# Kernel optimization log

Measured on AMD Instinct MI355X. Metric: run time of the kernel, lower is better.

The kernel has to match this reference:

```python
import jax, jax.numpy as jnp
import numpy as np

BLOCK = (4, 8, 8)   # (t, h, w)
NH, D, DA = 8, 512, 64
EPS = 1e-5


def _layernorm(x, g, b):
    m = jnp.mean(x, axis=-1, keepdims=True)
    xc = x - m
    v = jnp.mean(xc * xc, axis=-1, keepdims=True)
    return xc * jax.lax.rsqrt(v + EPS) * g + b


def setup_inputs() -> dict:
    key = jax.random.key(0)
    ks = jax.random.split(key, 10)
    B, T, H, W = 2, 8, 32, 32
    t, h, w = BLOCK
    s_qkv = (2.0 / (D + DA)) ** 0.5   # xavier_normal for (d, da) fan
    s_lin = (2.0 / (D + D)) ** 0.5
    return {
        "x": jax.random.normal(ks[0], (B, D, T, H, W), jnp.float32),
        "dt_bank": 0.02 * jax.random.normal(ks[1], (NH, 2 * t - 1), jnp.float32),
        "dh_bank": 0.02 * jax.random.normal(ks[2], (NH, 2 * h - 1), jnp.float32),
        "dw_bank": 0.02 * jax.random.normal(ks[3], (NH, 2 * w - 1), jnp.float32),
        "ln1_g": jnp.ones((D,), jnp.float32),
        "ln1_b": jnp.zeros((D,), jnp.float32),
        "w_q": s_qkv * jax.random.normal(ks[4], (NH, D, DA), jnp.float32),
        "w_k": s_qkv * jax.random.normal(ks[5], (NH, D, DA), jnp.float32),
        "w_v": s_qkv * jax.random.normal(ks[6], (NH, D, DA), jnp.float32),
        "w_proj": s_lin * jax.random.normal(ks[7], (D, NH * DA), jnp.float32),
        "ln2_g": jnp.ones((D,), jnp.float32),
        "ln2_b": jnp.zeros((D,), jnp.float32),
        "w1": s_lin * jax.random.normal(ks[8], (D, D), jnp.float32),
        "b1": jnp.zeros((D,), jnp.float32),
        "w2": s_lin * jax.random.normal(ks[9], (D, D), jnp.float32),
        "b2": jnp.zeros((D,), jnp.float32),
    }


def _axial_bias(dt_bank, dh_bank, dw_bank):
    t, h, w = BLOCK
    thw = t * h * w
    ar = jnp.arange(thw)
    tt = ar // (h * w)
    hh = (ar // w) % h
    ww = ar % w
    # relative offsets shifted to be non-negative (matches dt += abs(dt.min()))
    it = tt[:, None] - tt[None, :] + (t - 1)
    ih = hh[:, None] - hh[None, :] + (h - 1)
    iw = ww[:, None] - ww[None, :] + (w - 1)
    return dt_bank[:, it] + dh_bank[:, ih] + dw_bank[:, iw]  # (NH, thw, thw)


def reference(x, dt_bank, dh_bank, dw_bank, ln1_g, ln1_b, w_q, w_k, w_v,
              w_proj, ln2_g, ln2_b, w1, b1, w2, b2):
    B, C, T, H, W = x.shape
    t, h, w = BLOCK
    st, sh, sw = T // t, H // h, W // w
    thw = t * h * w
    nb = B * st * sh * sw

    # block split: (B,C,T,H,W) -> (nb, thw, C)
    xb = x.reshape(B, C, st, t, sh, h, sw, w).transpose(0, 2, 4, 6, 1, 3, 5, 7)
    xb = xb.reshape(nb, C, thw).transpose(0, 2, 1)

    Bb = _axial_bias(dt_bank, dh_bank, dw_bank)  # (NH, thw, thw)

    # --- multi-head attention with additive axial bias ---
    resid = xb
    xn = _layernorm(xb, ln1_g, ln1_b)
    q = jnp.einsum('bnd,hde->hbne', xn, w_q)
    k = jnp.einsum('bnd,hde->hbne', xn, w_k)
    v = jnp.einsum('bnd,hde->hbne', xn, w_v)
    scale = 1.0 / jnp.sqrt(jnp.asarray(DA, x.dtype))
    attn = jnp.einsum('hbne,hbme->hbnm', q, k) * scale + Bb[:, None]
    attn = jax.nn.softmax(attn, axis=-1)
    out = jnp.einsum('hbnm,hbme->hbne', attn, v)         # (NH, nb, thw, DA)
    out = out.transpose(1, 2, 0, 3).reshape(nb, thw, NH * DA)  # head-major concat
    out = out @ w_proj.T + resid

    # --- FFN with residual ---
    y = _layernorm(out, ln2_g, ln2_b)
    y = jax.nn.relu(y @ w1.T + b1) @ w2.T + b2
    out = y + out

    # un-block: (nb, thw, C) -> (B,C,T,H,W)
    out = out.transpose(0, 2, 1).reshape(B, st, sh, sw, C, t, h, w)
    out = out.transpose(0, 4, 1, 5, 2, 6, 3, 7).reshape(B, C, T, H, W)
    return out
```

## Files before the change

### kernel.cpp

```cpp
#include <hip/hip_runtime.h>
#include <hip/hip_bf16.h>
#include <stdint.h>

typedef __attribute__((ext_vector_type(4))) float f32x4;
typedef __attribute__((ext_vector_type(8))) short s16x8;
typedef __attribute__((ext_vector_type(4))) short s16x4;
typedef __attribute__((ext_vector_type(8))) __bf16 b16x8;

__device__ __forceinline__ f32x4 mfma16(s16x8 a, s16x8 b, f32x4 c) {
  return __builtin_amdgcn_mfma_f32_16x16x32_bf16(
      __builtin_bit_cast(b16x8, a), __builtin_bit_cast(b16x8, b), c, 0, 0, 0);
}

__device__ __forceinline__ void gl_lds16(const void* g, void* l) {
  __builtin_amdgcn_global_load_lds(
      (const __attribute__((address_space(1))) void*)g,
      (__attribute__((address_space(3))) void*)l, 16, 0, 0);
}

__device__ __forceinline__ unsigned short f2bf(float f) {
  union { float f; unsigned u; } v; v.f = f;
  unsigned u = v.u;
  return (unsigned short)((u + 0x7FFFu + ((u >> 16) & 1u)) >> 16);
}

__device__ __forceinline__ float bf2f(unsigned short u) {
  union { unsigned u; float f; } v; v.u = ((unsigned)u) << 16; return v.f;
}

__device__ __forceinline__ unsigned cvt_pk_bf16(float a, float b) {
  unsigned r;
  asm("v_cvt_pk_bf16_f32 %0, %1, %2" : "=v"(r) : "v"(a), "v"(b));
  return r;
}

#if __has_builtin(__builtin_amdgcn_exp2f)
#define EXP2F(x) __builtin_amdgcn_exp2f(x)
#else
#define EXP2F(x) exp2f(x)
#endif

__global__ __launch_bounds__(256) void k_prep(
    const float* __restrict__ wq, const float* __restrict__ wk, const float* __restrict__ wv,
    const float* __restrict__ wp, const float* __restrict__ w1, const float* __restrict__ w2,
    unsigned short* __restrict__ qkvT, unsigned short* __restrict__ wpT,
    unsigned short* __restrict__ w1T, unsigned short* __restrict__ w2T)
{
  int i = blockIdx.x * 256 + threadIdx.x;
  if (i < 786432) {
    int n = i >> 9, d = i & 511;
    const float* src = (n < 512) ? wq : (n < 1024 ? wk : wv);
    int nn = n & 511;
    int h = nn >> 6, e = nn & 63;
    qkvT[i] = f2bf(src[((size_t)h * 512 + d) * 64 + e]);
  } else {
    int j = i - 786432;
    int w = j >> 18;
    int o = j & 262143;
    const float* s = (w == 0) ? wp : (w == 1 ? w1 : w2);
    unsigned short* dst = (w == 0) ? wpT : (w == 1 ? w1T : w2T);
    dst[o] = f2bf(s[o]);
  }
}

__global__ __launch_bounds__(256) void k_gather_ln(
    const float* __restrict__ x, const float* __restrict__ g1, const float* __restrict__ b1,
    float* __restrict__ xb, unsigned short* __restrict__ xn)
{
  __shared__ float lx[16][517];
  int gid = blockIdx.x;
  int h2 = gid & 1, hh = (gid >> 1) & 7, tt = (gid >> 4) & 3,
      shI = (gid >> 6) & 3, stI = (gid >> 8) & 1, bI = (gid >> 9) & 1;
  const float* xbase = x + (size_t)bI * 4194304 + (size_t)(stI * 4 + tt) * 1024
                       + (shI * 8 + hh) * 32 + h2 * 16;
  int t = threadIdx.x;
  for (int i = 0; i < 8; ++i) {
    int slot = i * 256 + t;
    int c = slot >> 2, w8 = slot & 3;
    const float4 v = *(const float4*)(xbase + (size_t)c * 8192 + w8 * 4);
    lx[w8 * 4 + 0][c] = v.x; lx[w8 * 4 + 1][c] = v.y;
    lx[w8 * 4 + 2][c] = v.z; lx[w8 * 4 + 3][c] = v.w;
  }
  __syncthreads();
  int lane = t & 63, wid = t >> 6;
  for (int q = 0; q < 4; ++q) {
    int widx = wid * 4 + q;
    float vv[8]; float s = 0.f, ss = 0.f;
    #pragma unroll
    for (int i = 0; i < 8; ++i) { float v = lx[widx][lane + i * 64]; vv[i] = v; s += v; ss += v * v; }
    #pragma unroll
    for (int d = 1; d < 64; d <<= 1) { s += __shfl_xor(s, d); ss += __shfl_xor(ss, d); }
    float mean = s * (1.f / 512.f);
    float var = ss * (1.f / 512.f) - mean * mean;
    float rs = rsqrtf(var + 1e-5f);
    int sw = h2 * 2 + (widx >> 3), ww = widx & 7;
    int blk = ((bI * 2 + stI) * 4 + shI) * 4 + sw;
    int n = tt * 64 + hh * 8 + ww;
    size_t base = ((size_t)blk * 256 + n) * 512;
    #pragma unroll
    for (int i = 0; i < 8; ++i) {
      int c = lane + i * 64;
      float v = vv[i];
      xb[base + c] = v;
      xn[base + c] = f2bf((v - mean) * rs * g1[c] + b1[c]);
    }
  }
}

template<int EPI>
__global__ __launch_bounds__(256, 2) void k_gemm(
    const unsigned short* __restrict__ A, const unsigned short* __restrict__ Bt,
    int M, int N,
    unsigned short* __restrict__ Cbf, float* __restrict__ Cf,
    const float* __restrict__ bias, const float* __restrict__ addf,
    const unsigned short* __restrict__ addbf,
    unsigned short* __restrict__ vTout)
{
  constexpr int K = 512;
  __shared__ __align__(16) unsigned short a_lds[128 * 64];
  __shared__ __align__(16) unsigned short b_lds[128 * 64];
  int tid = threadIdx.x, lane = tid & 63, wid = tid >> 6;
  int lin = blockIdx.y * gridDim.x + blockIdx.x;
  int xcd = lin & 7, idx = lin >> 3;
  int bx = xcd * 16 + (idx & 15);
  int by = idx >> 4;
  int m0 = bx * 128, n0 = by * 128;
  int wm = (wid >> 1) * 64, wn = (wid & 1) * 64;
  int r15 = lane & 15, g = lane >> 4;

  f32x4 acc[4][4] = {};

  for (int ks = 0; ks < K; ks += 64) {
    #pragma unroll
    for (int s = 0; s < 4; ++s) {
      int seg = wid * 4 + s;
      int slot = seg * 64 + lane;
      int m = slot >> 3, lc = (slot & 7) ^ (m & 7);
      gl_lds16(A + (size_t)(m0 + m) * K + ks + lc * 8, (char*)a_lds + seg * 1024);
      gl_lds16(Bt + (size_t)(n0 + m) * K + ks + lc * 8, (char*)b_lds + seg * 1024);
    }
    __syncthreads();
    #pragma unroll
    for (int kk = 0; kk < 2; ++kk) {
      s16x8 af[4], bfr[4];
      #pragma unroll
      for (int f = 0; f < 4; ++f) {
        int mm = wm + f * 16 + r15;
        af[f] = *(const s16x8*)((const char*)a_lds + mm * 128 + (((kk * 4 + g) ^ (mm & 7)) * 16));
        int nn = wn + f * 16 + r15;
        bfr[f] = *(const s16x8*)((const char*)b_lds + nn * 128 + (((kk * 4 + g) ^ (nn & 7)) * 16));
      }
      __builtin_amdgcn_s_setprio(1);
      #pragma unroll
      for (int fm = 0; fm < 4; ++fm)
        #pragma unroll
        for (int fn = 0; fn < 4; ++fn)
          acc[fm][fn] = mfma16(af[fm], bfr[fn], acc[fm][fn]);
      __builtin_amdgcn_s_setprio(0);
    }
    __syncthreads();
  }

  int g4 = g * 4;
  #pragma unroll
  for (int fm = 0; fm < 4; ++fm) {
    #pragma unroll
    for (int fn = 0; fn < 4; ++fn) {
      int col = n0 + wn + fn * 16 + r15;
      int row0 = m0 + wm + fm * 16 + g4;
      if (EPI == 0 && col >= 1024) {
        int h = (col - 1024) >> 6, e = col & 63;
        int blk = row0 >> 8, mtok = row0 & 255;
        s16x4 pk;
        #pragma unroll
        for (int r = 0; r < 4; ++r) pk[r] = (short)f2bf(acc[fm][fn][r]);
        *(s16x4*)(vTout + (((size_t)blk * 8 + h) * 64 + e) * 256 + mtok) = pk;
      } else {
        #pragma unroll
        for (int r = 0; r < 4; ++r) {
          int row = row0 + r;
          float v = acc[fm][fn][r];
          if (EPI == 0) {
            Cbf[(size_t)row * 1536 + col] = f2bf(v);
          } else if (EPI == 1) {
            Cbf[(size_t)row * 512 + col] = f2bf(v + addf[(size_t)row * 512 + col]);
          } else if (EPI == 2) {
            Cbf[(size_t)row * 512 + col] = f2bf(fmaxf(v + bias[col], 0.f));
          } else {
            Cf[(size_t)row * 512 + col] = v + bias[col] + bf2f(addbf[(size_t)row * 512 + col]);
          }
        }
      }
    }
  }
}

__global__ __launch_bounds__(256, 1) void k_attn(
    const unsigned short* __restrict__ qkv, const unsigned short* __restrict__ vT,
    const float* __restrict__ dtb, const float* __restrict__ dhb, const float* __restrict__ dwb,
    unsigned short* __restrict__ aout)
{
  __shared__ __align__(16) unsigned short k_lds[2][64 * 64];
  __shared__ __align__(16) unsigned short v_lds[2][64 * 64];
  __shared__ __align__(16) unsigned short p_lds[4][64 * 64];
  __shared__ float bt_s[8], bh_s[16], bw_s[16];

  const float L2E = 1.44269504f;
  const float SC = 0.125f * 1.44269504f;

  int tid = threadIdx.x, lane = tid & 63, wid = tid >> 6;
  int bk = blockIdx.x >> 3, h = blockIdx.x & 7;
  if (tid < 7) bt_s[tid] = dtb[h * 7 + tid] * L2E;
  else if (tid < 22) bh_s[tid - 7] = dhb[h * 15 + tid - 7] * L2E;
  else if (tid < 37) bw_s[tid - 22] = dwb[h * 15 + tid - 22] * L2E;

  int r15 = lane & 15, g = lane >> 4;
  int wq0 = wid * 64;
  size_t bkBase = (size_t)bk * 256;
  const unsigned short* kbase = qkv + 512 + h * 64;
  const unsigned short* vbase = vT + ((size_t)bk * 8 + h) * 64 * 256;

  s16x8 qf[4][2];
  #pragma unroll
  for (int fn = 0; fn < 4; ++fn)
    #pragma unroll
    for (int kk = 0; kk < 2; ++kk)
      qf[fn][kk] = *(const s16x8*)(qkv + (bkBase + wq0 + fn * 16 + r15) * 1536
                                   + h * 64 + kk * 32 + g * 8);

  float btoff[4], hb[7], wb[4];

  #pragma unroll
  for (int s = 0; s < 4; ++s) {
    int sg = wid * 4 + s;
    if (sg < 8) {
      int slot = sg * 64 + lane;
      int m = slot >> 3, lc = (slot & 7) ^ (m & 7);
      gl_lds16(kbase + (bkBase + m) * 1536 + lc * 8, (char*)(&k_lds[0][0]) + sg * 1024);
    } else {
      int sg2 = sg - 8;
      int slot = sg2 * 64 + lane;
      int e = slot >> 3, lc = (slot & 7) ^ (e & 7);
      gl_lds16(vbase + (size_t)e * 256 + lc * 8, (char*)(&v_lds[0][0]) + sg2 * 1024);
    }
  }
  __syncthreads();

  {
    int Dh = (r15 >> 3) - (g >> 1) + 7;
    int Wb = (r15 & 7) - 4 * (g & 1) + 7;
    #pragma unroll
    for (int mt = 0; mt < 4; ++mt) btoff[mt] = bt_s[wid + 3 - mt];
    #pragma unroll
    for (int d = 0; d < 7; ++d) hb[d] = bh_s[Dh + 2 * d - 6];
    #pragma unroll
    for (int r = 0; r < 4; ++r) wb[r] = bw_s[Wb - r];
  }

  f32x4 o[4][4] = {};
  float mrun[4] = {-1e30f, -1e30f, -1e30f, -1e30f};
  float lrun[4] = {0.f, 0.f, 0.f, 0.f};
  char* p_w = (char*)(&p_lds[wid][0]);

  #pragma unroll
  for (int mt = 0; mt < 4; ++mt) {
    int cur = mt & 1;
    if (mt < 3) {
      int m0n = (mt + 1) * 64;
      #pragma unroll
      for (int s = 0; s < 4; ++s) {
        int sg = wid * 4 + s;
        if (sg < 8) {
          int slot = sg * 64 + lane;
          int m = slot >> 3, lc = (slot & 7) ^ (m & 7);
          gl_lds16(kbase + (bkBase + m0n + m) * 1536 + lc * 8,
                   (char*)(&k_lds[cur ^ 1][0]) + sg * 1024);
        } else {
          int sg2 = sg - 8;
          int slot = sg2 * 64 + lane;
          int e = slot >> 3, lc = (slot & 7) ^ (e & 7);
          gl_lds16(vbase + (size_t)e * 256 + m0n + lc * 8,
                   (char*)(&v_lds[cur ^ 1][0]) + sg2 * 1024);
        }
      }
    }
    const char* kl = (const char*)(&k_lds[cur][0]);
    const char* vl = (const char*)(&v_lds[cur][0]);

    f32x4 st[4][4] = {};
    #pragma unroll
    for (int kk = 0; kk < 2; ++kk) {
      s16x8 kf[4];
      #pragma unroll
      for (int fm = 0; fm < 4; ++fm) {
        int m = fm * 16 + r15;
        kf[fm] = *(const s16x8*)(kl + m * 128 + (((kk * 4 + g) ^ (m & 7)) * 16));
      }
      __builtin_amdgcn_s_setprio(1);
      #pragma unroll
      for (int fm = 0; fm < 4; ++fm)
        #pragma unroll
        for (int fn = 0; fn < 4; ++fn)
          st[fm][fn] = mfma16(kf[fm], qf[fn][kk], st[fm][fn]);
      __builtin_amdgcn_s_setprio(0);
    }

    #pragma unroll
    for (int fn = 0; fn < 4; ++fn) {
      float vals[16];
      float mx = -1e30f;
      #pragma unroll
      for (int fm = 0; fm < 4; ++fm) {
        float cc = btoff[mt] + hb[fn - fm + 3];
        #pragma unroll
        for (int r = 0; r < 4; ++r) {
          float v = fmaf(st[fm][fn][r], SC, cc) + wb[r];
          vals[fm * 4 + r] = v;
          mx = fmaxf(mx, v);
        }
      }
      mx = fmaxf(mx, __shfl_xor(mx, 16));
      mx = fmaxf(mx, __shfl_xor(mx, 32));
      if (!__all(mx <= mrun[fn] + 8.f)) {
        float mnew = fmaxf(mrun[fn], mx);
        float al = EXP2F(mrun[fn] - mnew);
        mrun[fn] = mnew;
        lrun[fn] *= al;
        #pragma unroll
        for (int fe = 0; fe < 4; ++fe)
          #pragma unroll
          for (int r = 0; r < 4; ++r)
            o[fe][fn][r] *= al;
      }
      float m_c = mrun[fn];
      float p[16]; float sum = 0.f;
      #pragma unroll
      for (int i = 0; i < 16; ++i) { p[i] = EXP2F(vals[i] - m_c); sum += p[i]; }
      sum += __shfl_xor(sum, 16);
      sum += __shfl_xor(sum, 32);
      lrun[fn] += sum;
      int nl = fn * 16 + r15;
      char* prow = p_w + nl * 128 + (g & 1) * 8;
      #pragma unroll
      for (int fm = 0; fm < 4; ++fm) {
        unsigned u0 = cvt_pk_bf16(p[fm * 4 + 0], p[fm * 4 + 1]);
        unsigned u1 = cvt_pk_bf16(p[fm * 4 + 2], p[fm * 4 + 3]);
        int lc = fm * 2 + (g >> 1);
        *(uint2*)(prow + ((lc ^ (nl & 7)) * 16)) = make_uint2(u0, u1);
      }
    }
    asm volatile("s_waitcnt lgkmcnt(0)" ::: "memory");

    #pragma unroll
    for (int mm = 0; mm < 2; ++mm) {
      s16x8 vf[4], pf[4];
      #pragma unroll
      for (int fe = 0; fe < 4; ++fe) {
        int e = fe * 16 + r15;
        vf[fe] = *(const s16x8*)(vl + e * 128 + (((mm * 4 + g) ^ (e & 7)) * 16));
      }
      #pragma unroll
      for (int fn = 0; fn < 4; ++fn) {
        int nl = fn * 16 + r15;
        pf[fn] = *(const s16x8*)(p_w + nl * 128 + (((mm * 4 + g) ^ (nl & 7)) * 16));
      }
      __builtin_amdgcn_s_setprio(1);
      #pragma unroll
      for (int fe = 0; fe < 4; ++fe)
        #pragma unroll
        for (int fn = 0; fn < 4; ++fn)
          o[fe][fn] = mfma16(vf[fe][0] ? vf[fe] : vf[fe], pf[fn], o[fe][fn]);
      __builtin_amdgcn_s_setprio(0);
    }
    __syncthreads();
  }

  #pragma unroll
  for (int fn = 0; fn < 4; ++fn) {
    float inv = 1.f / lrun[fn];
    size_t rowb = (bkBase + wq0 + fn * 16 + r15) * 512 + h * 64;
    #pragma unroll
    for (int fe = 0; fe < 4; ++fe) {
      unsigned u0 = cvt_pk_bf16(o[fe][fn][0] * inv, o[fe][fn][1] * inv);
      unsigned u1 = cvt_pk_bf16(o[fe][fn][2] * inv, o[fe][fn][3] * inv);
      *(uint2*)(aout + rowb + fe * 16 + g * 4) = make_uint2(u0, u1);
    }
  }
}

__global__ __launch_bounds__(256) void k_ln2(
    const unsigned short* __restrict__ in, const float* __restrict__ g2, const float* __restrict__ b2,
    unsigned short* __restrict__ out)
{
  int token = blockIdx.x * 4 + (threadIdx.x >> 6);
  int lane = threadIdx.x & 63;
  s16x8 v8 = *(const s16x8*)(in + (size_t)token * 512 + lane * 8);
  float vv[8]; float s = 0.f, ss = 0.f;
  #pragma unroll
  for (int i = 0; i < 8; ++i) {
    float v = bf2f((unsigned short)v8[i]); vv[i] = v; s += v; ss += v * v;
  }
  #pragma unroll
  for (int d = 1; d < 64; d <<= 1) { s += __shfl_xor(s, d); ss += __shfl_xor(ss, d); }
  float mean = s * (1.f / 512.f);
  float var = ss * (1.f / 512.f) - mean * mean;
  float rs = rsqrtf(var + 1e-5f);
  const float4 gA = *(const float4*)(g2 + lane * 8);
  const float4 gB = *(const float4*)(g2 + lane * 8 + 4);
  const float4 bA = *(const float4*)(b2 + lane * 8);
  const float4 bB = *(const float4*)(b2 + lane * 8 + 4);
  float gv[8] = {gA.x, gA.y, gA.z, gA.w, gB.x, gB.y, gB.z, gB.w};
  float bv[8] = {bA.x, bA.y, bA.z, bA.w, bB.x, bB.y, bB.z, bB.w};
  s16x8 o8;
  #pragma unroll
  for (int i = 0; i < 8; ++i)
    o8[i] = (short)f2bf((vv[i] - mean) * rs * gv[i] + bv[i]);
  *(s16x8*)(out + (size_t)token * 512 + lane * 8) = o8;
}

__global__ __launch_bounds__(64) void k_scatter(
    const float* __restrict__ fin, float* __restrict__ out)
{
  __shared__ float lx[32][33];
  int gid = blockIdx.x;
  int cc = gid & 15;
  int sg = gid >> 4;
  int hh = sg & 7, tt = (sg >> 3) & 3, shI = (sg >> 5) & 3, stI = (sg >> 7) & 1, bI = (sg >> 8) & 1;
  int c0 = cc * 32;
  int l = threadIdx.x;
  #pragma unroll
  for (int i = 0; i < 4; ++i) {
    int slot = i * 64 + l;
    int tok = slot >> 3, c4 = slot & 7;
    int blk = ((bI * 2 + stI) * 4 + shI) * 4 + (tok >> 3);
    int n = tt * 64 + hh * 8 + (tok & 7);
    const float4 v = *(const float4*)(fin + ((size_t)blk * 256 + n) * 512 + c0 + c4 * 4);
    lx[tok][c4 * 4 + 0] = v.x; lx[tok][c4 * 4 + 1] = v.y;
    lx[tok][c4 * 4 + 2] = v.z; lx[tok][c4 * 4 + 3] = v.w;
  }
  __syncthreads();
  size_t obase = (size_t)bI * 4194304 + (size_t)(stI * 4 + tt) * 1024 + (shI * 8 + hh) * 32;
  #pragma unroll
  for (int i = 0; i < 4; ++i) {
    int crow = i * 8 + (l >> 3), w4 = l & 7;
    float4 v;
    v.x = lx[w4 * 4 + 0][crow]; v.y = lx[w4 * 4 + 1][crow];
    v.z = lx[w4 * 4 + 2][crow]; v.w = lx[w4 * 4 + 3][crow];
    *(float4*)(out + obase + (size_t)(c0 + crow) * 8192 + w4 * 4) = v;
  }
}

extern "C" void kernel_launch(void* const* d_in, const int* in_sizes, int n_in,
                              void* d_out, int out_size, void* d_ws, size_t ws_size,
                              hipStream_t stream)
{
  const float* x   = (const float*)d_in[0];
  const float* dtb = (const float*)d_in[1];
  const float* dhb = (const float*)d_in[2];
  const float* dwb = (const float*)d_in[3];
  const float* g1  = (const float*)d_in[4];
  const float* bb1 = (const float*)d_in[5];
  const float* wq  = (const float*)d_in[6];
  const float* wk  = (const float*)d_in[7];
  const float* wv  = (const float*)d_in[8];
  const float* wp  = (const float*)d_in[9];
  const float* g2  = (const float*)d_in[10];
  const float* bb2 = (const float*)d_in[11];
  const float* w1  = (const float*)d_in[12];
  const float* fb1 = (const float*)d_in[13];
  const float* w2  = (const float*)d_in[14];
  const float* fb2 = (const float*)d_in[15];

  char* ws = (char*)d_ws;
  float*          xb   = (float*)(ws + 0);
  unsigned short* vT   = (unsigned short*)(ws + 33554432);
  unsigned short* out1b= (unsigned short*)(ws + 33554432);
  unsigned short* qkv  = (unsigned short*)(ws + 67108864);
  unsigned short* xn   = (unsigned short*)(ws + 117440512);
  unsigned short* qkvT = (unsigned short*)(ws + 134217728);
  unsigned short* wpT  = (unsigned short*)(ws + 135790592);
  unsigned short* w1T  = (unsigned short*)(ws + 136314880);
  unsigned short* w2T  = (unsigned short*)(ws + 136839168);

  unsigned short* attn_out = xn;
  unsigned short* yb = xn;
  unsigned short* h1 = qkv;
  float* finalb = xb;
  float* outp = (float*)d_out;

  k_prep<<<6144, 256, 0, stream>>>(wq, wk, wv, wp, w1, w2, qkvT, wpT, w1T, w2T);
  k_gather_ln<<<1024, 256, 0, stream>>>(x, g1, bb1, xb, xn);
  k_gemm<0><<<dim3(128, 12), 256, 0, stream>>>(xn, qkvT, 16384, 1536, qkv, nullptr, nullptr, nullptr, nullptr, vT);
  k_attn<<<512, 256, 0, stream>>>(qkv, vT, dtb, dhb, dwb, attn_out);
  k_gemm<1><<<dim3(128, 4), 256, 0, stream>>>(attn_out, wpT, 16384, 512, out1b, nullptr, nullptr, xb, nullptr, nullptr);
  k_ln2<<<4096, 256, 0, stream>>>(out1b, g2, bb2, yb);
  k_gemm<2><<<dim3(128, 4), 256, 0, stream>>>(yb, w1T, 16384, 512, h1, nullptr, fb1, nullptr, nullptr, nullptr);
  k_gemm<3><<<dim3(128, 4), 256, 0, stream>>>(h1, w2T, 16384, 512, nullptr, finalb, fb2, nullptr, out1b, nullptr);
  k_scatter<<<8192, 64, 0, stream>>>(finalb, outp);
}
```

Before: 168.3 us.

## Double-buffer GEMM LDS tiles, store residual as bf16, fuse weight prep into gather

```diff
diff --git a/kernel.cpp b/kernel.cpp
--- a/kernel.cpp
+++ b/kernel.cpp
@@ -40,33 +40,32 @@
 #define EXP2F(x) exp2f(x)
 #endif
 
-__global__ __launch_bounds__(256) void k_prep(
+__global__ __launch_bounds__(256) void k_gather_ln(
+    const float* __restrict__ x, const float* __restrict__ g1, const float* __restrict__ b1,
+    unsigned short* __restrict__ xb, unsigned short* __restrict__ xn,
     const float* __restrict__ wq, const float* __restrict__ wk, const float* __restrict__ wv,
     const float* __restrict__ wp, const float* __restrict__ w1, const float* __restrict__ w2,
     unsigned short* __restrict__ qkvT, unsigned short* __restrict__ wpT,
     unsigned short* __restrict__ w1T, unsigned short* __restrict__ w2T)
 {
-  int i = blockIdx.x * 256 + threadIdx.x;
-  if (i < 786432) {
-    int n = i >> 9, d = i & 511;
-    const float* src = (n < 512) ? wq : (n < 1024 ? wk : wv);
-    int nn = n & 511;
-    int h = nn >> 6, e = nn & 63;
-    qkvT[i] = f2bf(src[((size_t)h * 512 + d) * 64 + e]);
-  } else {
-    int j = i - 786432;
-    int w = j >> 18;
-    int o = j & 262143;
-    const float* s = (w == 0) ? wp : (w == 1 ? w1 : w2);
-    unsigned short* dst = (w == 0) ? wpT : (w == 1 ? w1T : w2T);
-    dst[o] = f2bf(s[o]);
-  }
-}
-
-__global__ __launch_bounds__(256) void k_gather_ln(
-    const float* __restrict__ x, const float* __restrict__ g1, const float* __restrict__ b1,
-    float* __restrict__ xb, unsigned short* __restrict__ xn)
-{
+  if (blockIdx.x >= 1024) {
+    int i = (blockIdx.x - 1024) * 256 + threadIdx.x;
+    if (i < 786432) {
+      int n = i >> 9, d = i & 511;
+      const float* src = (n < 512) ? wq : (n < 1024 ? wk : wv);
+      int nn = n & 511;
+      int h = nn >> 6, e = nn & 63;
+      qkvT[i] = f2bf(src[((size_t)h * 512 + d) * 64 + e]);
+    } else {
+      int j = i - 786432;
+      int w = j >> 18;
+      int o = j & 262143;
+      const float* s = (w == 0) ? wp : (w == 1 ? w1 : w2);
+      unsigned short* dst = (w == 0) ? wpT : (w == 1 ? w1T : w2T);
+      dst[o] = f2bf(s[o]);
+    }
+    return;
+  }
   __shared__ float lx[16][517];
   int gid = blockIdx.x;
   int h2 = gid & 1, hh = (gid >> 1) & 7, tt = (gid >> 4) & 3,
@@ -101,7 +100,7 @@
     for (int i = 0; i < 8; ++i) {
       int c = lane + i * 64;
       float v = vv[i];
-      xb[base + c] = v;
+      xb[base + c] = f2bf(v);
       xn[base + c] = f2bf((v - mean) * rs * g1[c] + b1[c]);
     }
   }
@@ -112,13 +111,13 @@
     const unsigned short* __restrict__ A, const unsigned short* __restrict__ Bt,
     int M, int N,
     unsigned short* __restrict__ Cbf, float* __restrict__ Cf,
-    const float* __restrict__ bias, const float* __restrict__ addf,
+    const float* __restrict__ bias,
     const unsigned short* __restrict__ addbf,
     unsigned short* __restrict__ vTout)
 {
   constexpr int K = 512;
-  __shared__ __align__(16) unsigned short a_lds[128 * 64];
-  __shared__ __align__(16) unsigned short b_lds[128 * 64];
+  __shared__ __align__(16) unsigned short a_lds[2][128 * 64];
+  __shared__ __align__(16) unsigned short b_lds[2][128 * 64];
   int tid = threadIdx.x, lane = tid & 63, wid = tid >> 6;
   int lin = blockIdx.y * gridDim.x + blockIdx.x;
   int xcd = lin & 7, idx = lin >> 3;
@@ -128,27 +127,49 @@
   int wm = (wid >> 1) * 64, wn = (wid & 1) * 64;
   int r15 = lane & 15, g = lane >> 4;
 
+  const unsigned short* aptr[4];
+  const unsigned short* bptr[4];
+  int segoff[4];
+  #pragma unroll
+  for (int s = 0; s < 4; ++s) {
+    int seg = wid * 4 + s;
+    int slot = seg * 64 + lane;
+    int m = slot >> 3, lc = (slot & 7) ^ (m & 7);
+    aptr[s] = A + (size_t)(m0 + m) * K + lc * 8;
+    bptr[s] = Bt + (size_t)(n0 + m) * K + lc * 8;
+    segoff[s] = seg * 1024;
+  }
+
   f32x4 acc[4][4] = {};
 
-  for (int ks = 0; ks < K; ks += 64) {
-    #pragma unroll
-    for (int s = 0; s < 4; ++s) {
-      int seg = wid * 4 + s;
-      int slot = seg * 64 + lane;
-      int m = slot >> 3, lc = (slot & 7) ^ (m & 7);
-      gl_lds16(A + (size_t)(m0 + m) * K + ks + lc * 8, (char*)a_lds + seg * 1024);
-      gl_lds16(Bt + (size_t)(n0 + m) * K + ks + lc * 8, (char*)b_lds + seg * 1024);
-    }
-    __syncthreads();
+  #pragma unroll
+  for (int s = 0; s < 4; ++s) {
+    gl_lds16(aptr[s], (char*)a_lds[0] + segoff[s]);
+    gl_lds16(bptr[s], (char*)b_lds[0] + segoff[s]);
+  }
+  __syncthreads();
+
+  for (int it = 0; it < 8; ++it) {
+    int cur = it & 1;
+    if (it < 7) {
+      int ksn = (it + 1) * 64;
+      #pragma unroll
+      for (int s = 0; s < 4; ++s) {
+        gl_lds16(aptr[s] + ksn, (char*)a_lds[cur ^ 1] + segoff[s]);
+        gl_lds16(bptr[s] + ksn, (char*)b_lds[cur ^ 1] + segoff[s]);
+      }
+    }
+    const char* al = (const char*)a_lds[cur];
+    const char* bl = (const char*)b_lds[cur];
     #pragma unroll
     for (int kk = 0; kk < 2; ++kk) {
       s16x8 af[4], bfr[4];
       #pragma unroll
       for (int f = 0; f < 4; ++f) {
         int mm = wm + f * 16 + r15;
-        af[f] = *(const s16x8*)((const char*)a_lds + mm * 128 + (((kk * 4 + g) ^ (mm & 7)) * 16));
+        af[f] = *(const s16x8*)(al + mm * 128 + (((kk * 4 + g) ^ (mm & 7)) * 16));
         int nn = wn + f * 16 + r15;
-        bfr[f] = *(const s16x8*)((const char*)b_lds + nn * 128 + (((kk * 4 + g) ^ (nn & 7)) * 16));
+        bfr[f] = *(const s16x8*)(bl + nn * 128 + (((kk * 4 + g) ^ (nn & 7)) * 16));
       }
       __builtin_amdgcn_s_setprio(1);
       #pragma unroll
@@ -183,7 +204,7 @@
           if (EPI == 0) {
             Cbf[(size_t)row * 1536 + col] = f2bf(v);
           } else if (EPI == 1) {
-            Cbf[(size_t)row * 512 + col] = f2bf(v + addf[(size_t)row * 512 + col]);
+            Cbf[(size_t)row * 512 + col] = f2bf(v + bf2f(addbf[(size_t)row * 512 + col]));
           } else if (EPI == 2) {
             Cbf[(size_t)row * 512 + col] = f2bf(fmaxf(v + bias[col], 0.f));
           } else {
@@ -369,7 +390,7 @@
       for (int fe = 0; fe < 4; ++fe)
         #pragma unroll
         for (int fn = 0; fn < 4; ++fn)
-          o[fe][fn] = mfma16(vf[fe][0] ? vf[fe] : vf[fe], pf[fn], o[fe][fn]);
+          o[fe][fn] = mfma16(vf[fe], pf[fn], o[fe][fn]);
       __builtin_amdgcn_s_setprio(0);
     }
     __syncthreads();
@@ -472,7 +493,8 @@
   const float* fb2 = (const float*)d_in[15];
 
   char* ws = (char*)d_ws;
-  float*          xb   = (float*)(ws + 0);
+  unsigned short* xb   = (unsigned short*)(ws + 0);
+  float*          finalb = (float*)(ws + 0);
   unsigned short* vT   = (unsigned short*)(ws + 33554432);
   unsigned short* out1b= (unsigned short*)(ws + 33554432);
   unsigned short* qkv  = (unsigned short*)(ws + 67108864);
@@ -485,16 +507,15 @@
   unsigned short* attn_out = xn;
   unsigned short* yb = xn;
   unsigned short* h1 = qkv;
-  float* finalb = xb;
   float* outp = (float*)d_out;
 
-  k_prep<<<6144, 256, 0, stream>>>(wq, wk, wv, wp, w1, w2, qkvT, wpT, w1T, w2T);
-  k_gather_ln<<<1024, 256, 0, stream>>>(x, g1, bb1, xb, xn);
-  k_gemm<0><<<dim3(128, 12), 256, 0, stream>>>(xn, qkvT, 16384, 1536, qkv, nullptr, nullptr, nullptr, nullptr, vT);
+  k_gather_ln<<<1024 + 6144, 256, 0, stream>>>(x, g1, bb1, xb, xn,
+      wq, wk, wv, wp, w1, w2, qkvT, wpT, w1T, w2T);
+  k_gemm<0><<<dim3(128, 12), 256, 0, stream>>>(xn, qkvT, 16384, 1536, qkv, nullptr, nullptr, nullptr, vT);
   k_attn<<<512, 256, 0, stream>>>(qkv, vT, dtb, dhb, dwb, attn_out);
-  k_gemm<1><<<dim3(128, 4), 256, 0, stream>>>(attn_out, wpT, 16384, 512, out1b, nullptr, nullptr, xb, nullptr, nullptr);
+  k_gemm<1><<<dim3(128, 4), 256, 0, stream>>>(attn_out, wpT, 16384, 512, out1b, nullptr, nullptr, xb, nullptr);
   k_ln2<<<4096, 256, 0, stream>>>(out1b, g2, bb2, yb);
-  k_gemm<2><<<dim3(128, 4), 256, 0, stream>>>(yb, w1T, 16384, 512, h1, nullptr, fb1, nullptr, nullptr, nullptr);
-  k_gemm<3><<<dim3(128, 4), 256, 0, stream>>>(h1, w2T, 16384, 512, nullptr, finalb, fb2, nullptr, out1b, nullptr);
+  k_gemm<2><<<dim3(128, 4), 256, 0, stream>>>(yb, w1T, 16384, 512, h1, nullptr, fb1, nullptr, nullptr);
+  k_gemm<3><<<dim3(128, 4), 256, 0, stream>>>(h1, w2T, 16384, 512, nullptr, finalb, fb2, out1b, nullptr);
   k_scatter<<<8192, 64, 0, stream>>>(finalb, outp);
 }
```

Result: faster. 157.1 us (-6.6%).
